# Optimization experiments

Hardware: AMD Instinct MI355X
Metric: run time of the kernel (lower is better)

Reference implementation:

```python
import jax, jax.numpy as jnp
import numpy as np

IGNORE_INDEX = -100


def setup_inputs() -> dict:
    key = jax.random.key(0)
    k1, k2 = jax.random.split(key)
    logits = jax.random.normal(k1, (8, 19, 512, 512), dtype=jnp.float32)
    labels = jax.random.randint(k2, (8, 512, 512), 0, 19, dtype=jnp.int64)
    return {"logits": logits, "labels": labels}


def reference(logits, labels):
    # Lovasz-Softmax loss (CoinCheung/pytorch-loss LovaszSoftmaxV3, reduction='mean').
    n, c, h, w = logits.shape
    lg = jnp.moveaxis(logits, 1, 0).reshape(c, -1).astype(jnp.float32)  # [C, P]
    lb = labels.reshape(-1)  # [P]
    valid = (lb != IGNORE_INDEX)

    probs = jax.nn.softmax(lg, axis=0)  # [C, P]
    # one-hot labels, zeroed at ignored pixels
    onehot = ((jnp.arange(c)[:, None] == lb[None, :]) & valid[None, :]).astype(jnp.float32)

    errs = jnp.abs(onehot - probs)
    # push ignored pixels to the end of the descending sort with sentinel -1
    errs = jnp.where(valid[None, :], errs, jnp.float32(-1.0))

    order = jnp.argsort(-errs, axis=1)  # descending sort per class
    errs_sort = jnp.take_along_axis(errs, order, axis=1)
    oh_sort = jnp.take_along_axis(onehot, order, axis=1)

    # Lovasz extension gradient (jacc), computed without autodiff flow
    n_pos = oh_sort.sum(axis=1, keepdims=True)
    inter = n_pos - jnp.cumsum(oh_sort, axis=1)
    union = n_pos + jnp.cumsum(1.0 - oh_sort, axis=1)
    jacc = 1.0 - inter / union
    jacc = jnp.concatenate([jacc[:, :1], jacc[:, 1:] - jacc[:, :-1]], axis=1)

    # ignored pixels have errs_sort = -1 -> relu zeroes their contribution
    losses = jnp.sum(jax.nn.relu(errs_sort) * jacc, axis=1)  # per-class [C]
    return losses.mean()
```

## Files before the change

kernel.cpp:

```cpp
#include <hip/hip_runtime.h>
#include <hip/hip_bf16.h>

#define NCLASS 19
#define BINS 512
#define NB (NCLASS * BINS)
#define NREP 4
#define RPAD 8
#define RSTRIDE (NB + RPAD)
#define IGNORE_IDX (-100)
#define HW_SHIFT 18
#define HW_C (1 << HW_SHIFT)

#define UNPACK(v)                                            \
  (((unsigned long long)((v) >> 16) << 32) |                 \
   (unsigned long long)((v) & 0xffffu))

#define LOADSET(V, LB, PIX)                                                  \
  {                                                                          \
    int n_ = (PIX) >> HW_SHIFT;                                              \
    int hw_ = (PIX) & (HW_C - 1);                                            \
    const float* lp_ =                                                       \
        logits + (((size_t)n_ * NCLASS) << HW_SHIFT) + hw_;                  \
    _Pragma("unroll") for (int c_ = 0; c_ < NCLASS; ++c_) {                  \
      float2 q_ = *(const float2*)(lp_ + ((size_t)c_ << HW_SHIFT));          \
      V[c_][0] = q_.x;                                                       \
      V[c_][1] = q_.y;                                                       \
    }                                                                        \
    LB = *(const int2*)(labels + (PIX));                                     \
  }

#define PROCSET(V, LB)                                                       \
  {                                                                          \
    float m0_ = -3.4e38f, m1_ = -3.4e38f;                                    \
    _Pragma("unroll") for (int c_ = 0; c_ < NCLASS; ++c_) {                  \
      m0_ = fmaxf(m0_, V[c_][0]);                                            \
      m1_ = fmaxf(m1_, V[c_][1]);                                            \
    }                                                                        \
    float s0_ = 0.f, s1_ = 0.f;                                              \
    _Pragma("unroll") for (int c_ = 0; c_ < NCLASS; ++c_) {                  \
      V[c_][0] = __expf(V[c_][0] - m0_); s0_ += V[c_][0];                    \
      V[c_][1] = __expf(V[c_][1] - m1_); s1_ += V[c_][1];                    \
    }                                                                        \
    float i0_ = 1.0f / s0_, i1_ = 1.0f / s1_;                                \
    int l0_ = LB.x, l1_ = LB.y;                                              \
    _Pragma("unroll") for (int c_ = 0; c_ < NCLASS; ++c_) {                  \
      if (l0_ != IGNORE_IDX) {                                               \
        float pr_ = V[c_][0] * i0_;                                          \
        bool pos_ = (c_ == l0_);                                             \
        float e_ = pos_ ? (1.0f - pr_) : pr_;                                \
        int b_ = min(BINS - 1, (int)(e_ * (float)BINS));                     \
        atomicAdd(&sh[rep + (c_ << 9) + b_], pos_ ? 0x10000u : 1u);          \
      }                                                                      \
      if (l1_ != IGNORE_IDX) {                                               \
        float pr_ = V[c_][1] * i1_;                                          \
        bool pos_ = (c_ == l1_);                                             \
        float e_ = pos_ ? (1.0f - pr_) : pr_;                                \
        int b_ = min(BINS - 1, (int)(e_ * (float)BINS));                     \
        atomicAdd(&sh[rep + (c_ << 9) + b_], pos_ ? 0x10000u : 1u);          \
      }                                                                      \
    }                                                                        \
  }

__global__ void __launch_bounds__(1024, 4) hist_pf(
    const float* __restrict__ logits, const int* __restrict__ labels,
    unsigned* __restrict__ copies, unsigned* __restrict__ counter, int P,
    int ppb) {
  extern __shared__ unsigned sh[];
  if (blockIdx.x == 0 && threadIdx.x == 0) *counter = 0u;
  for (int i = threadIdx.x; i < NREP * RSTRIDE; i += 1024) sh[i] = 0u;
  __syncthreads();

  const int rep = (threadIdx.x & 3) * RSTRIDE;
  const int STEP = 1024 * 2;
  int p1 = min(P, blockIdx.x * ppb + ppb);
  int p = blockIdx.x * ppb + (int)threadIdx.x * 2;

  float va[NCLASS][2], vb[NCLASS][2];
  int2 la, lb;
  bool has = p < p1;
  if (has) LOADSET(va, la, p);
  while (has) {
    int pn = p + STEP;
    bool hasn = pn < p1;
    if (hasn) LOADSET(vb, lb, pn);
    PROCSET(va, la);
    p = pn;
    has = hasn;
    if (!has) break;
    pn = p + STEP;
    hasn = pn < p1;
    if (hasn) LOADSET(va, la, pn);
    PROCSET(vb, lb);
    p = pn;
    has = hasn;
  }
  __syncthreads();

  unsigned* dst = copies + (size_t)blockIdx.x * NB;
  for (int i = threadIdx.x; i < NB; i += 1024)
    dst[i] =
        sh[i] + sh[RSTRIDE + i] + sh[2 * RSTRIDE + i] + sh[3 * RSTRIDE + i];
}

__global__ void __launch_bounds__(1024) scan19_fused(
    const unsigned* __restrict__ copies, float* __restrict__ partial,
    unsigned* __restrict__ counter, float* __restrict__ out, int R) {
  int c = blockIdx.x;
  __shared__ unsigned long long binsA[BINS];
  __shared__ unsigned long long binsB[BINS];
  __shared__ float fsum[16];
  int tid = threadIdx.x;
  int bin = tid & (BINS - 1);
  int half = tid >> 9;

  int hc = R >> 1;
  int r0 = half * hc;
  const unsigned* base = copies + (c << 9) + bin;
  unsigned long long a0 = 0, a1 = 0, a2 = 0, a3 = 0, a4 = 0, a5 = 0, a6 = 0,
                     a7 = 0;
  for (int r = 0; r < hc; r += 8) {
    unsigned v0 = base[(size_t)(r0 + r + 0) * NB];
    unsigned v1 = base[(size_t)(r0 + r + 1) * NB];
    unsigned v2 = base[(size_t)(r0 + r + 2) * NB];
    unsigned v3 = base[(size_t)(r0 + r + 3) * NB];
    unsigned v4 = base[(size_t)(r0 + r + 4) * NB];
    unsigned v5 = base[(size_t)(r0 + r + 5) * NB];
    unsigned v6 = base[(size_t)(r0 + r + 6) * NB];
    unsigned v7 = base[(size_t)(r0 + r + 7) * NB];
    a0 += UNPACK(v0);
    a1 += UNPACK(v1);
    a2 += UNPACK(v2);
    a3 += UNPACK(v3);
    a4 += UNPACK(v4);
    a5 += UNPACK(v5);
    a6 += UNPACK(v6);
    a7 += UNPACK(v7);
  }
  unsigned long long a = ((a0 + a1) + (a2 + a3)) + ((a4 + a5) + (a6 + a7));
  if (half == 0)
    binsA[bin] = a;
  else
    binsB[bin] = a;
  __syncthreads();
  if (half == 0) binsA[bin] += binsB[bin];
  __syncthreads();

  for (int off = 1; off < BINS; off <<= 1) {
    unsigned long long add = 0;
    if (half == 0 && bin + off < BINS) add = binsA[bin + off];
    __syncthreads();
    if (half == 0) binsA[bin] += add;
    __syncthreads();
  }

  float nPos = (float)(unsigned)(binsA[0] >> 32);
  float acc = 0.f;
  if (half == 0 && bin >= 1) {
    unsigned long long suff = binsA[bin];
    float CP = (float)(unsigned)(suff >> 32);
    float CN = (float)(unsigned)(suff & 0xffffffffull);
    float uni = nPos + CN;
    if (uni > 0.f) acc = 1.0f - (nPos - CP) / uni;
  }

  for (int off = 32; off > 0; off >>= 1) acc += __shfl_down(acc, off, 64);
  int lane = tid & 63, w = tid >> 6;
  if (lane == 0) fsum[w] = acc;
  __syncthreads();
  if (tid == 0) {
    float t = 0.f;
#pragma unroll
    for (int i = 0; i < 16; ++i) t += fsum[i];
    partial[c] = t;
    __threadfence();
    unsigned tk = atomicAdd(counter, 1u);
    if (tk == NCLASS - 1) {
      __threadfence();
      float m = 0.f;
#pragma unroll
      for (int i = 0; i < NCLASS; ++i)
        m += __hip_atomic_load(&partial[i], __ATOMIC_RELAXED,
                               __HIP_MEMORY_SCOPE_AGENT);
      out[0] = m * (1.0f / ((float)BINS * (float)NCLASS));
    }
  }
}

extern "C" void kernel_launch(void* const* d_in, const int* in_sizes, int n_in,
                              void* d_out, int out_size, void* d_ws,
                              size_t ws_size, hipStream_t stream) {
  const float* logits = (const float*)d_in[0];
  const int* labels = (const int*)d_in[1];
  float* out = (float*)d_out;

  const int P = in_sizes[1];

  int R = 256;
  while (R > 32 && (size_t)R * NB * 4 + 4096 > ws_size) R >>= 1;
  int ppb = ((P + R - 1) / R + 2047) & ~2047;

  char* ws = (char*)d_ws;
  unsigned* copies = (unsigned*)ws;
  float* partial = (float*)(ws + (size_t)R * NB * 4);
  unsigned* counter = (unsigned*)(partial + 32);

  size_t ldsBytes = (size_t)NREP * RSTRIDE * 4;

  hist_pf<<<R, 1024, ldsBytes, stream>>>(logits, labels, copies, counter, P,
                                         ppb);
  scan19_fused<<<NCLASS, 1024, 0, stream>>>(copies, partial, counter, out, R);
}
```

Measured before the change: 48.82 us.

## Split per-class histogram reduction across eight slices with last-block finalization

```diff
diff --git a/kernel.cpp b/kernel.cpp
--- a/kernel.cpp
+++ b/kernel.cpp
@@ -7,6 +7,7 @@
 #define NREP 4
 #define RPAD 8
 #define RSTRIDE (NB + RPAD)
+#define NSLICE 8
 #define IGNORE_IDX (-100)
 #define HW_SHIFT 18
 #define HW_C (1 << HW_SHIFT)
@@ -63,10 +64,10 @@
 
 __global__ void __launch_bounds__(1024, 4) hist_pf(
     const float* __restrict__ logits, const int* __restrict__ labels,
-    unsigned* __restrict__ copies, unsigned* __restrict__ counter, int P,
+    unsigned* __restrict__ copies, unsigned* __restrict__ counters, int P,
     int ppb) {
   extern __shared__ unsigned sh[];
-  if (blockIdx.x == 0 && threadIdx.x == 0) *counter = 0u;
+  if (blockIdx.x == 0 && threadIdx.x < NCLASS + 1) counters[threadIdx.x] = 0u;
   for (int i = threadIdx.x; i < NREP * RSTRIDE; i += 1024) sh[i] = 0u;
   __syncthreads();
 
@@ -102,47 +103,62 @@
         sh[i] + sh[RSTRIDE + i] + sh[2 * RSTRIDE + i] + sh[3 * RSTRIDE + i];
 }
 
-__global__ void __launch_bounds__(1024) scan19_fused(
-    const unsigned* __restrict__ copies, float* __restrict__ partial,
-    unsigned* __restrict__ counter, float* __restrict__ out, int R) {
-  int c = blockIdx.x;
+__global__ void __launch_bounds__(1024) scan19_split(
+    const unsigned* __restrict__ copies, unsigned long long* __restrict__ partS,
+    float* __restrict__ partial, unsigned* __restrict__ counters,
+    float* __restrict__ out, int R) {
+  int c = blockIdx.x >> 3;
+  int s = blockIdx.x & (NSLICE - 1);
+  int tid = threadIdx.x;
+  int bin = tid & (BINS - 1);
+  int half = tid >> 9;
+
   __shared__ unsigned long long binsA[BINS];
   __shared__ unsigned long long binsB[BINS];
   __shared__ float fsum[16];
-  int tid = threadIdx.x;
-  int bin = tid & (BINS - 1);
-  int half = tid >> 9;
-
-  int hc = R >> 1;
-  int r0 = half * hc;
+  __shared__ unsigned tk_sh;
+
+  int spc = R >> 3;
+  int hc = spc >> 1;
+  int r0 = s * spc + half * hc;
   const unsigned* base = copies + (c << 9) + bin;
-  unsigned long long a0 = 0, a1 = 0, a2 = 0, a3 = 0, a4 = 0, a5 = 0, a6 = 0,
-                     a7 = 0;
-  for (int r = 0; r < hc; r += 8) {
+  unsigned long long a0 = 0, a1 = 0, a2 = 0, a3 = 0;
+  for (int r = 0; r < hc; r += 4) {
     unsigned v0 = base[(size_t)(r0 + r + 0) * NB];
     unsigned v1 = base[(size_t)(r0 + r + 1) * NB];
     unsigned v2 = base[(size_t)(r0 + r + 2) * NB];
     unsigned v3 = base[(size_t)(r0 + r + 3) * NB];
-    unsigned v4 = base[(size_t)(r0 + r + 4) * NB];
-    unsigned v5 = base[(size_t)(r0 + r + 5) * NB];
-    unsigned v6 = base[(size_t)(r0 + r + 6) * NB];
-    unsigned v7 = base[(size_t)(r0 + r + 7) * NB];
     a0 += UNPACK(v0);
     a1 += UNPACK(v1);
     a2 += UNPACK(v2);
     a3 += UNPACK(v3);
-    a4 += UNPACK(v4);
-    a5 += UNPACK(v5);
-    a6 += UNPACK(v6);
-    a7 += UNPACK(v7);
-  }
-  unsigned long long a = ((a0 + a1) + (a2 + a3)) + ((a4 + a5) + (a6 + a7));
+  }
+  unsigned long long a = (a0 + a1) + (a2 + a3);
   if (half == 0)
     binsA[bin] = a;
   else
     binsB[bin] = a;
   __syncthreads();
   if (half == 0) binsA[bin] += binsB[bin];
+  __syncthreads();
+
+  if (tid < BINS) partS[((size_t)blockIdx.x << 9) + tid] = binsA[tid];
+
+  __threadfence();
+  __syncthreads();
+  if (tid == 0) tk_sh = atomicAdd(&counters[c], 1u);
+  __syncthreads();
+  if (tk_sh != NSLICE - 1) return;
+
+  __threadfence();
+  if (tid < BINS) {
+    unsigned long long t = 0;
+#pragma unroll
+    for (int i = 0; i < NSLICE; ++i)
+      t += __hip_atomic_load(&partS[(((size_t)(c << 3) + i) << 9) + tid],
+                             __ATOMIC_RELAXED, __HIP_MEMORY_SCOPE_AGENT);
+    binsA[tid] = t;
+  }
   __syncthreads();
 
   for (int off = 1; off < BINS; off <<= 1) {
@@ -173,7 +189,7 @@
     for (int i = 0; i < 16; ++i) t += fsum[i];
     partial[c] = t;
     __threadfence();
-    unsigned tk = atomicAdd(counter, 1u);
+    unsigned tk = atomicAdd(&counters[NCLASS], 1u);
     if (tk == NCLASS - 1) {
       __threadfence();
       float m = 0.f;
@@ -196,17 +212,23 @@
   const int P = in_sizes[1];
 
   int R = 256;
-  while (R > 32 && (size_t)R * NB * 4 + 4096 > ws_size) R >>= 1;
+  while (R > 64 &&
+         (size_t)R * NB * 4 + (size_t)NCLASS * NSLICE * BINS * 8 + 4096 >
+             ws_size)
+    R >>= 1;
   int ppb = ((P + R - 1) / R + 2047) & ~2047;
 
   char* ws = (char*)d_ws;
   unsigned* copies = (unsigned*)ws;
-  float* partial = (float*)(ws + (size_t)R * NB * 4);
-  unsigned* counter = (unsigned*)(partial + 32);
+  unsigned long long* partS =
+      (unsigned long long*)(ws + (size_t)R * NB * 4);
+  float* partial = (float*)(partS + (size_t)NCLASS * NSLICE * BINS);
+  unsigned* counters = (unsigned*)(partial + 32);
 
   size_t ldsBytes = (size_t)NREP * RSTRIDE * 4;
 
-  hist_pf<<<R, 1024, ldsBytes, stream>>>(logits, labels, copies, counter, P,
+  hist_pf<<<R, 1024, ldsBytes, stream>>>(logits, labels, copies, counters, P,
                                          ppb);
-  scan19_fused<<<NCLASS, 1024, 0, stream>>>(copies, partial, counter, out, R);
+  scan19_split<<<NCLASS * NSLICE, 1024, 0, stream>>>(copies, partS, partial,
+                                                     counters, out, R);
 }
```

New measurement: 108.4 us. 122% more time.

## Merge per-block histograms with global 64-bit atomics instead of per-block copies

Applied to the files above, without the earlier changes.

```diff
diff --git a/kernel.cpp b/kernel.cpp
--- a/kernel.cpp
+++ b/kernel.cpp
@@ -63,10 +63,8 @@
 
 __global__ void __launch_bounds__(1024, 4) hist_pf(
     const float* __restrict__ logits, const int* __restrict__ labels,
-    unsigned* __restrict__ copies, unsigned* __restrict__ counter, int P,
-    int ppb) {
+    unsigned long long* __restrict__ hist, int P, int ppb) {
   extern __shared__ unsigned sh[];
-  if (blockIdx.x == 0 && threadIdx.x == 0) *counter = 0u;
   for (int i = threadIdx.x; i < NREP * RSTRIDE; i += 1024) sh[i] = 0u;
   __syncthreads();
 
@@ -96,67 +94,35 @@
   }
   __syncthreads();
 
-  unsigned* dst = copies + (size_t)blockIdx.x * NB;
-  for (int i = threadIdx.x; i < NB; i += 1024)
-    dst[i] =
+  for (int i = threadIdx.x; i < NB; i += 1024) {
+    unsigned t =
         sh[i] + sh[RSTRIDE + i] + sh[2 * RSTRIDE + i] + sh[3 * RSTRIDE + i];
+    atomicAdd(&hist[i], UNPACK(t));
+  }
 }
 
-__global__ void __launch_bounds__(1024) scan19_fused(
-    const unsigned* __restrict__ copies, float* __restrict__ partial,
-    unsigned* __restrict__ counter, float* __restrict__ out, int R) {
+__global__ void __launch_bounds__(512) scan19_hist(
+    const unsigned long long* __restrict__ hist, float* __restrict__ partial,
+    unsigned* __restrict__ counter, float* __restrict__ out) {
   int c = blockIdx.x;
   __shared__ unsigned long long binsA[BINS];
-  __shared__ unsigned long long binsB[BINS];
-  __shared__ float fsum[16];
+  __shared__ float fsum[8];
   int tid = threadIdx.x;
-  int bin = tid & (BINS - 1);
-  int half = tid >> 9;
 
-  int hc = R >> 1;
-  int r0 = half * hc;
-  const unsigned* base = copies + (c << 9) + bin;
-  unsigned long long a0 = 0, a1 = 0, a2 = 0, a3 = 0, a4 = 0, a5 = 0, a6 = 0,
-                     a7 = 0;
-  for (int r = 0; r < hc; r += 8) {
-    unsigned v0 = base[(size_t)(r0 + r + 0) * NB];
-    unsigned v1 = base[(size_t)(r0 + r + 1) * NB];
-    unsigned v2 = base[(size_t)(r0 + r + 2) * NB];
-    unsigned v3 = base[(size_t)(r0 + r + 3) * NB];
-    unsigned v4 = base[(size_t)(r0 + r + 4) * NB];
-    unsigned v5 = base[(size_t)(r0 + r + 5) * NB];
-    unsigned v6 = base[(size_t)(r0 + r + 6) * NB];
-    unsigned v7 = base[(size_t)(r0 + r + 7) * NB];
-    a0 += UNPACK(v0);
-    a1 += UNPACK(v1);
-    a2 += UNPACK(v2);
-    a3 += UNPACK(v3);
-    a4 += UNPACK(v4);
-    a5 += UNPACK(v5);
-    a6 += UNPACK(v6);
-    a7 += UNPACK(v7);
-  }
-  unsigned long long a = ((a0 + a1) + (a2 + a3)) + ((a4 + a5) + (a6 + a7));
-  if (half == 0)
-    binsA[bin] = a;
-  else
-    binsB[bin] = a;
-  __syncthreads();
-  if (half == 0) binsA[bin] += binsB[bin];
+  binsA[tid] = hist[(c << 9) + tid];
   __syncthreads();
 
   for (int off = 1; off < BINS; off <<= 1) {
-    unsigned long long add = 0;
-    if (half == 0 && bin + off < BINS) add = binsA[bin + off];
+    unsigned long long add = (tid + off < BINS) ? binsA[tid + off] : 0ull;
     __syncthreads();
-    if (half == 0) binsA[bin] += add;
+    binsA[tid] += add;
     __syncthreads();
   }
 
   float nPos = (float)(unsigned)(binsA[0] >> 32);
   float acc = 0.f;
-  if (half == 0 && bin >= 1) {
-    unsigned long long suff = binsA[bin];
+  if (tid >= 1) {
+    unsigned long long suff = binsA[tid];
     float CP = (float)(unsigned)(suff >> 32);
     float CN = (float)(unsigned)(suff & 0xffffffffull);
     float uni = nPos + CN;
@@ -170,7 +136,7 @@
   if (tid == 0) {
     float t = 0.f;
 #pragma unroll
-    for (int i = 0; i < 16; ++i) t += fsum[i];
+    for (int i = 0; i < 8; ++i) t += fsum[i];
     partial[c] = t;
     __threadfence();
     unsigned tk = atomicAdd(counter, 1u);
@@ -195,18 +161,18 @@
 
   const int P = in_sizes[1];
 
-  int R = 256;
-  while (R > 32 && (size_t)R * NB * 4 + 4096 > ws_size) R >>= 1;
+  const int R = 256;
   int ppb = ((P + R - 1) / R + 2047) & ~2047;
 
   char* ws = (char*)d_ws;
-  unsigned* copies = (unsigned*)ws;
-  float* partial = (float*)(ws + (size_t)R * NB * 4);
-  unsigned* counter = (unsigned*)(partial + 32);
+  unsigned long long* hist = (unsigned long long*)ws;
+  unsigned* counter = (unsigned*)(ws + (size_t)NB * 8);
+  float* partial = (float*)(counter + 16);
 
   size_t ldsBytes = (size_t)NREP * RSTRIDE * 4;
 
-  hist_pf<<<R, 1024, ldsBytes, stream>>>(logits, labels, copies, counter, P,
-                                         ppb);
-  scan19_fused<<<NCLASS, 1024, 0, stream>>>(copies, partial, counter, out, R);
+  hipMemsetAsync(ws, 0, (size_t)NB * 8 + 64, stream);
+
+  hist_pf<<<R, 1024, ldsBytes, stream>>>(logits, labels, hist, P, ppb);
+  scan19_hist<<<NCLASS, 512, 0, stream>>>(hist, partial, counter, out);
 }
```

Result: slower. 59.35 us (+21.6%).
